# Performance work log

Hardware: AMD Instinct MI355X
Metric: run time of the kernel (lower is better)

Reference implementation:

```python
import jax, jax.numpy as jnp
import numpy as np

N, H, W, C = 8, 64, 64, 256
G, KS = 4, 3
K = KS * KS                      # 9 kernel points (remove_center=False)
GD = C // G                      # 64 channels per group
OM_DIM = int(np.ceil(G * K * 3 / 8) * 8)   # 112 = offsets(72)+mask(36)+pad(4)
STRIDE = PAD = DIL = 1
OFFSET_SCALE = 1.0
SOFTMAX = False


def setup_inputs() -> dict:
    ks = jax.random.split(jax.random.key(0), 6)
    s = 0.02
    return {
        "x": jax.random.normal(ks[0], (N, H * W, C), jnp.float32),
        "shape_h": H,
        "shape_w": W,
        "w_in": jax.random.normal(ks[1], (C, C), jnp.float32) * s,
        "b_in": jnp.zeros((C,), jnp.float32),
        "w_out": jax.random.normal(ks[2], (C, C), jnp.float32) * s,
        "b_out": jnp.zeros((C,), jnp.float32),
        "w_dw": jax.random.normal(ks[3], (KS, KS, 1, C), jnp.float32) * s,  # depthwise HWIO
        "b_dw": jnp.zeros((C,), jnp.float32),
        "w_pw": jax.random.normal(ks[4], (OM_DIM, C), jnp.float32) * s,
        "b_pw": jnp.zeros((OM_DIM,), jnp.float32),
    }


def _deform_sample(xg, px, py, mask):
    # xg: [N, H*W, G, GD]; px/py/mask: [N, H, W, G, K]
    # Bilinear sample with zero padding outside the image, mask-weighted sum over K.
    n_idx = jnp.arange(N)[:, None, None, None, None]
    g_idx = jnp.arange(G)[None, None, None, :, None]
    x0 = jnp.floor(px)
    y0 = jnp.floor(py)
    out = jnp.zeros((N, H, W, G, GD), xg.dtype)
    for dy in (0, 1):
        for dx in (0, 1):
            xi = x0 + dx
            yi = y0 + dy
            wgt = (1.0 - jnp.abs(px - xi)) * (1.0 - jnp.abs(py - yi))
            valid = (xi >= 0) & (xi <= W - 1) & (yi >= 0) & (yi <= H - 1)
            wgt = jnp.where(valid, wgt, 0.0) * mask                     # [N,H,W,G,K]
            flat = (jnp.clip(yi, 0, H - 1) * W + jnp.clip(xi, 0, W - 1)).astype(jnp.int32)
            vals = xg[n_idx, flat, g_idx, :]                            # [N,H,W,G,K,GD]
            out = out + jnp.einsum("nhwgk,nhwgkc->nhwgc", wgt, vals)
    return out


def _forward(x, w_in, b_in, w_out, b_out, w_dw, b_dw, w_pw, b_pw):
    out = x @ w_in.T + b_in                                             # proj_input [N,L,C]
    # offset/mask branch runs on the raw (unprojected) input
    dw = jax.lax.conv_general_dilated(
        x.reshape(N, H, W, C), w_dw, (1, 1), [(PAD, PAD), (PAD, PAD)],
        dimension_numbers=("NHWC", "HWIO", "NHWC"), feature_group_count=C) + b_dw
    om = (dw.reshape(N, H * W, C) @ w_pw.T + b_pw).reshape(N, H, W, OM_DIM)
    off = om[..., : 2 * G * K].reshape(N, H, W, G, K, 2)                # (dx, dy)
    mask = om[..., 2 * G * K : 3 * G * K].reshape(N, H, W, G, K)
    if SOFTMAX:
        mask = jax.nn.softmax(mask, axis=-1)
    # sampling locations in input pixel coordinates (DCNv3 reference points)
    kk = (jnp.arange(KS) - (KS - 1) // 2) * DIL
    kgy, kgx = jnp.meshgrid(kk, kk, indexing="ij")
    kgx = kgx.reshape(-1).astype(x.dtype)                               # [K]
    kgy = kgy.reshape(-1).astype(x.dtype)
    base = (DIL * (KS - 1)) // 2 - PAD
    bx = (jnp.arange(W) * STRIDE + base).astype(x.dtype)
    by = (jnp.arange(H) * STRIDE + base).astype(x.dtype)
    px = bx[None, None, :, None, None] + OFFSET_SCALE * (kgx + off[..., 0])
    py = by[None, :, None, None, None] + OFFSET_SCALE * (kgy + off[..., 1])
    samp = _deform_sample(out.reshape(N, H * W, G, GD), px, py, mask)   # [N,H,W,G,GD]
    return samp.reshape(N, H * W, C) @ w_out.T + b_out                  # proj_output


def reference(x, shape_h, shape_w, w_in, b_in, w_out, b_out, w_dw, b_dw, w_pw, b_pw):
    assert (shape_h, shape_w) == (H, W)
    return _forward(x, w_in, b_in, w_out, b_out, w_dw, b_dw, w_pw, b_pw)
```

## Files before the change

kernel.cpp:

```cpp
#include <hip/hip_runtime.h>

#define HW     4096
#define M_ROWS 32768
#define OMD    112
#define OMP    128

typedef __attribute__((ext_vector_type(8))) short short8;
typedef __attribute__((ext_vector_type(4))) float f32x4;

__device__ inline unsigned short f2bf(float f) {
  union { float f; unsigned int u; } v; v.f = f;
  unsigned int u = v.u;
  u += 0x7fffu + ((u >> 16) & 1u);
  return (unsigned short)(u >> 16);
}
__device__ inline float bf2f(unsigned short h) {
  union { unsigned int u; float f; } v; v.u = ((unsigned int)h) << 16;
  return v.f;
}

__global__ __launch_bounds__(256) void prep_fused(
    const float* __restrict__ x, const float* __restrict__ w_dw,
    const float* __restrict__ b_dw, const float* __restrict__ w_in,
    const float* __restrict__ w_out, const float* __restrict__ w_pw,
    const float* __restrict__ b_pw, unsigned short* __restrict__ xb,
    unsigned short* __restrict__ dwb, unsigned short* __restrict__ wi_b,
    unsigned short* __restrict__ wo_b, unsigned short* __restrict__ wp_b,
    float* __restrict__ bpw_pad) {
  int bid = blockIdx.x;
  int tid = threadIdx.x;
  if (bid < 8192) {
    int idx = bid * 256 + tid;
    int c4 = (idx & 63) * 4;
    int pp = idx >> 6;
    int n = pp >> 12;
    int hw = pp & 4095;
    int h = hw >> 6, w = hw & 63;
    float4 bb = *(const float4*)&b_dw[c4];
    float a0 = bb.x, a1 = bb.y, a2 = bb.z, a3 = bb.w;
#pragma unroll
    for (int ky = 0; ky < 3; ++ky) {
      int iy = h + ky - 1;
      if (iy < 0 || iy > 63) continue;
#pragma unroll
      for (int kx = 0; kx < 3; ++kx) {
        int ix = w + kx - 1;
        if (ix < 0 || ix > 63) continue;
        float4 xv = *(const float4*)&x[((size_t)(n << 12) + iy * 64 + ix) * 256 + c4];
        float4 wv = *(const float4*)&w_dw[(ky * 3 + kx) * 256 + c4];
        a0 += xv.x * wv.x;
        a1 += xv.y * wv.y;
        a2 += xv.z * wv.z;
        a3 += xv.w * wv.w;
      }
    }
    ushort4 o;
    o.x = f2bf(a0); o.y = f2bf(a1); o.z = f2bf(a2); o.w = f2bf(a3);
    *(ushort4*)&dwb[(size_t)pp * 256 + c4] = o;
    float4 cv = *(const float4*)&x[(size_t)pp * 256 + c4];
    ushort4 oc;
    oc.x = f2bf(cv.x); oc.y = f2bf(cv.y); oc.z = f2bf(cv.z); oc.w = f2bf(cv.w);
    *(ushort4*)&xb[(size_t)pp * 256 + c4] = oc;
  } else {
    int idx = (bid - 8192) * 256 + tid;
    if (idx < 65536) {
      wi_b[idx] = f2bf(w_in[idx]);
    } else if (idx < 131072) {
      int i = idx - 65536;
      wo_b[i] = f2bf(w_out[i]);
    } else if (idx < 131072 + OMP * 256) {
      int i = idx - 131072;
      int o = i >> 8;
      wp_b[i] = (o < OMD) ? f2bf(w_pw[i]) : (unsigned short)0;
    } else if (idx < 131072 + OMP * 256 + OMP) {
      int i = idx - (131072 + OMP * 256);
      bpw_pad[i] = (i < OMD) ? b_pw[i] : 0.f;
    }
  }
}

__global__ __launch_bounds__(256) void gemm_mid(
    const unsigned short* __restrict__ dwb, const unsigned short* __restrict__ wp_b,
    const float* __restrict__ bpw, unsigned short* __restrict__ om,
    const unsigned short* __restrict__ xb, const unsigned short* __restrict__ wi_b,
    const float* __restrict__ b_in, unsigned short* __restrict__ vproj) {
  __shared__ __align__(16) unsigned short As[128 * 32];
  __shared__ __align__(16) unsigned short Bs[128 * 32];
  int tid = threadIdx.x;
  int wave = tid >> 6, lane = tid & 63;
  int wr = wave >> 1, wc = wave & 1;

  const unsigned short *A, *W;
  const float* bias;
  unsigned short* Cout;
  int NN, colB;
  size_t rowB;
  int bid = blockIdx.x;
  if (bid < 256) {
    int swz = (bid & 7) * 32 + (bid >> 3);
    A = dwb; W = wp_b; bias = bpw; Cout = om; NN = 128;
    rowB = (size_t)swz * 128; colB = 0;
  } else {
    int b = bid - 256;
    int swz = (b & 7) * 64 + (b >> 3);
    A = xb; W = wi_b; bias = b_in; Cout = vproj; NN = 256;
    rowB = (size_t)(swz >> 1) * 128; colB = (swz & 1) * 128;
  }

  f32x4 acc[4][4];
#pragma unroll
  for (int m = 0; m < 4; ++m)
#pragma unroll
    for (int n = 0; n < 4; ++n) acc[m][n] = (f32x4)(0.f);

  int arow = lane >> 2;
  int acol = (lane & 3) * 8;

  for (int k0 = 0; k0 < 256; k0 += 32) {
#pragma unroll
    for (int jj = 0; jj < 2; ++jj) {
      int j = wave * 2 + jj;
      const unsigned short* ga = A + (rowB + 16 * j + arow) * 256 + k0 + acol;
      __builtin_amdgcn_global_load_lds(
          (const __attribute__((address_space(1))) unsigned int*)ga,
          (__attribute__((address_space(3))) unsigned int*)(As + j * 512),
          16, 0, 0);
      const unsigned short* gb =
          W + ((size_t)(colB + 16 * j + arow)) * 256 + k0 + acol;
      __builtin_amdgcn_global_load_lds(
          (const __attribute__((address_space(1))) unsigned int*)gb,
          (__attribute__((address_space(3))) unsigned int*)(Bs + j * 512),
          16, 0, 0);
    }
    __syncthreads();

    short8 aF[4], bF[4];
#pragma unroll
    for (int m = 0; m < 4; ++m)
      aF[m] = *(const short8*)&As[(wr * 64 + m * 16 + (lane & 15)) * 32 +
                                  (lane >> 4) * 8];
#pragma unroll
    for (int n = 0; n < 4; ++n)
      bF[n] = *(const short8*)&Bs[(wc * 64 + n * 16 + (lane & 15)) * 32 +
                                  (lane >> 4) * 8];
#pragma unroll
    for (int m = 0; m < 4; ++m)
#pragma unroll
      for (int n = 0; n < 4; ++n)
        acc[m][n] = __builtin_amdgcn_mfma_f32_16x16x32_bf16(
            aF[m], bF[n], acc[m][n], 0, 0, 0);
    __syncthreads();
  }

#pragma unroll
  for (int n = 0; n < 4; ++n) {
    int col = colB + wc * 64 + n * 16 + (lane & 15);
    float bv = bias[col];
#pragma unroll
    for (int m = 0; m < 4; ++m) {
#pragma unroll
      for (int j = 0; j < 4; ++j) {
        size_t row = rowB + wr * 64 + m * 16 + (lane >> 4) * 4 + j;
        Cout[row * NN + col] = f2bf(acc[m][n][j] + bv);
      }
    }
  }
}

__global__ __launch_bounds__(256) void gemm_out(
    const unsigned short* __restrict__ A, const unsigned short* __restrict__ W,
    const float* __restrict__ bias, float* __restrict__ Cout) {
  __shared__ __align__(16) unsigned short As[128 * 32];
  __shared__ __align__(16) unsigned short Bs[128 * 32];
  int tid = threadIdx.x;
  int wave = tid >> 6, lane = tid & 63;
  int wr = wave >> 1, wc = wave & 1;

  int bid = blockIdx.x;
  int swz = (bid & 7) * 64 + (bid >> 3);
  size_t rowB = (size_t)(swz >> 1) * 128;
  int colB = (swz & 1) * 128;

  f32x4 acc[4][4];
#pragma unroll
  for (int m = 0; m < 4; ++m)
#pragma unroll
    for (int n = 0; n < 4; ++n) acc[m][n] = (f32x4)(0.f);

  int arow = lane >> 2;
  int acol = (lane & 3) * 8;

  for (int k0 = 0; k0 < 256; k0 += 32) {
#pragma unroll
    for (int jj = 0; jj < 2; ++jj) {
      int j = wave * 2 + jj;
      const unsigned short* ga = A + (rowB + 16 * j + arow) * 256 + k0 + acol;
      __builtin_amdgcn_global_load_lds(
          (const __attribute__((address_space(1))) unsigned int*)ga,
          (__attribute__((address_space(3))) unsigned int*)(As + j * 512),
          16, 0, 0);
      const unsigned short* gb =
          W + ((size_t)(colB + 16 * j + arow)) * 256 + k0 + acol;
      __builtin_amdgcn_global_load_lds(
          (const __attribute__((address_space(1))) unsigned int*)gb,
          (__attribute__((address_space(3))) unsigned int*)(Bs + j * 512),
          16, 0, 0);
    }
    __syncthreads();

    short8 aF[4], bF[4];
#pragma unroll
    for (int m = 0; m < 4; ++m)
      aF[m] = *(const short8*)&As[(wr * 64 + m * 16 + (lane & 15)) * 32 +
                                  (lane >> 4) * 8];
#pragma unroll
    for (int n = 0; n < 4; ++n)
      bF[n] = *(const short8*)&Bs[(wc * 64 + n * 16 + (lane & 15)) * 32 +
                                  (lane >> 4) * 8];
#pragma unroll
    for (int m = 0; m < 4; ++m)
#pragma unroll
      for (int n = 0; n < 4; ++n)
        acc[m][n] = __builtin_amdgcn_mfma_f32_16x16x32_bf16(
            aF[m], bF[n], acc[m][n], 0, 0, 0);
    __syncthreads();
  }

#pragma unroll
  for (int n = 0; n < 4; ++n) {
    int col = colB + wc * 64 + n * 16 + (lane & 15);
    float bv = bias[col];
#pragma unroll
    for (int m = 0; m < 4; ++m) {
#pragma unroll
      for (int j = 0; j < 4; ++j) {
        size_t row = rowB + wr * 64 + m * 16 + (lane >> 4) * 4 + j;
        Cout[row * 256 + col] = acc[m][n][j] + bv;
      }
    }
  }
}

__global__ __launch_bounds__(256) void deform_sample_b3(
    const unsigned short* __restrict__ vproj, const unsigned short* __restrict__ om,
    unsigned short* __restrict__ samp) {
  int bid = blockIdx.x;
  int swz = (bid & 7) * 512 + (bid >> 3);
  int p0 = swz * 8;

  int tid = threadIdx.x;

  __shared__ __align__(16) float s_w[8][36][4];
  __shared__ __align__(16) int   s_o[8][36][4];

  for (int it = tid; it < 288; it += 256) {
    int pix = it / 36, gk = it % 36;
    int k = gk % 9;
    int p = p0 + pix;
    int h = (p >> 6) & 63, w = p & 63;
    const unsigned short* o = om + (size_t)p * OMP;
    float ox = bf2f(o[gk * 2]), oy = bf2f(o[gk * 2 + 1]);
    float m = bf2f(o[72 + gk]);
    float px = (float)(w + (k % 3) - 1) + ox;
    float py = (float)(h + (k / 3) - 1) + oy;
    float x0f = floorf(px), y0f = floorf(py);
    int x0 = (int)x0f, y0 = (int)y0f;
    float fx = px - x0f, fy = py - y0f;
    bool vx0 = (unsigned)x0 < 64u;
    bool vx1 = (unsigned)(x0 + 1) < 64u;
    bool vy0 = (unsigned)y0 < 64u;
    bool vy1 = (unsigned)(y0 + 1) < 64u;
    s_w[pix][gk][0] = (vy0 && vx0) ? (1.f - fx) * (1.f - fy) * m : 0.f;
    s_w[pix][gk][1] = (vy0 && vx1) ? fx * (1.f - fy) * m : 0.f;
    s_w[pix][gk][2] = (vy1 && vx0) ? (1.f - fx) * fy * m : 0.f;
    s_w[pix][gk][3] = (vy1 && vx1) ? fx * fy * m : 0.f;
    int x0c = min(max(x0, 0), 63), x1c = min(max(x0 + 1, 0), 63);
    int y0c = min(max(y0, 0), 63), y1c = min(max(y0 + 1, 0), 63);
    s_o[pix][gk][0] = (y0c * 64 + x0c) * 512;
    s_o[pix][gk][1] = (y0c * 64 + x1c) * 512;
    s_o[pix][gk][2] = (y1c * 64 + x0c) * 512;
    s_o[pix][gk][3] = (y1c * 64 + x1c) * 512;
  }
  __syncthreads();

  int wave = tid >> 6, lane = tid & 63;
  int pix2 = lane >> 5, sub = lane & 31, g = sub >> 3;
  int pixb = wave * 2 + pix2;
  int p = p0 + pixb;
  int n = p0 >> 12;
  const char* vb = (const char*)(vproj + (((size_t)n << 12)) * 256);
  int choff = sub * 16;

  float acc[8];
#pragma unroll
  for (int j = 0; j < 8; ++j) acc[j] = 0.f;

#pragma unroll
  for (int k = 0; k < 9; ++k) {
    int gk = g * 9 + k;
    float4 wv = *(const float4*)s_w[pixb][gk];
    int4 ov = *(const int4*)s_o[pixb][gk];
#pragma unroll
    for (int c = 0; c < 4; ++c) {
      int off = (c == 0) ? ov.x : (c == 1) ? ov.y : (c == 2) ? ov.z : ov.w;
      float wgt = (c == 0) ? wv.x : (c == 1) ? wv.y : (c == 2) ? wv.z : wv.w;
      short8 v = *(const short8*)(vb + off + choff);
#pragma unroll
      for (int j = 0; j < 8; ++j)
        acc[j] += wgt * bf2f((unsigned short)v[j]);
    }
  }

  union { unsigned short s[8]; short8 v8; } o;
#pragma unroll
  for (int j = 0; j < 8; ++j) o.s[j] = f2bf(acc[j]);
  *(short8*)&samp[(size_t)p * 256 + sub * 8] = o.v8;
}

extern "C" void kernel_launch(void* const* d_in, const int* in_sizes, int n_in,
                              void* d_out, int out_size, void* d_ws,
                              size_t ws_size, hipStream_t stream) {
  const float* x     = (const float*)d_in[0];
  const float* w_in  = (const float*)d_in[3];
  const float* b_in  = (const float*)d_in[4];
  const float* w_out = (const float*)d_in[5];
  const float* b_out = (const float*)d_in[6];
  const float* w_dw  = (const float*)d_in[7];
  const float* b_dw  = (const float*)d_in[8];
  const float* w_pw  = (const float*)d_in[9];
  const float* b_pw  = (const float*)d_in[10];
  float* out = (float*)d_out;
  char* ws = (char*)d_ws;

  unsigned short* xb    = (unsigned short*)(ws);
  unsigned short* dwb   = (unsigned short*)(ws + (16u << 20));
  unsigned short* vproj = (unsigned short*)(ws + (32u << 20));
  unsigned short* om    = (unsigned short*)(ws + (48u << 20));
  unsigned short* wi_b  = (unsigned short*)(ws + (56u << 20));
  unsigned short* wo_b  = (unsigned short*)(ws + (56u << 20) + (128u << 10));
  unsigned short* wp_b  = (unsigned short*)(ws + (56u << 20) + (256u << 10));
  float*          bpw   = (float*)(ws + (56u << 20) + (320u << 10));

  prep_fused<<<8834, 256, 0, stream>>>(x, w_dw, b_dw, w_in, w_out, w_pw, b_pw,
                                       xb, dwb, wi_b, wo_b, wp_b, bpw);
  gemm_mid<<<768, 256, 0, stream>>>(dwb, wp_b, bpw, om, xb, wi_b, b_in, vproj);
  deform_sample_b3<<<4096, 256, 0, stream>>>(vproj, om, dwb );
  gemm_out<<<512, 256, 0, stream>>>(dwb, wo_b, b_out, out);
}
```

Baseline: 80.81 us.

## Fuse deformable sampling into output projection GEMM via shared memory tile

Merges the bilinear deform-sampling kernel with the output projection GEMM. Each block samples 64 pixels into a padded LDS tile, then multiplies it against the full 256-column weight matrix with MFMA. This removes the bf16 round trip of the sampled tensor through global memory and one kernel launch. In exchange the grid shrinks to 512 blocks, the sampling phase has less parallelism per block, and every block reloads all of W.

```diff
diff --git a/kernel.cpp b/kernel.cpp
--- a/kernel.cpp
+++ b/kernel.cpp
@@ -167,43 +167,90 @@
   }
 }
 
-__global__ __launch_bounds__(256) void gemm_out(
-    const unsigned short* __restrict__ A, const unsigned short* __restrict__ W,
-    const float* __restrict__ bias, float* __restrict__ Cout) {
-  __shared__ __align__(16) unsigned short As[128 * 32];
-  __shared__ __align__(16) unsigned short Bs[128 * 32];
+__global__ __launch_bounds__(256) void fused_sample_gemm(
+    const unsigned short* __restrict__ vproj, const unsigned short* __restrict__ om,
+    const unsigned short* __restrict__ W, const float* __restrict__ bias,
+    float* __restrict__ out) {
+  constexpr int AP = 264;
+  __shared__ __align__(16) unsigned short As[64 * AP];
+  __shared__ __align__(16) unsigned short Bs[256 * 32];
+
+  int bid = blockIdx.x;
+  int swz = (bid & 7) * 64 + (bid >> 3);
+  int p0 = swz * 64;
+  int n = p0 >> 12;
+
   int tid = threadIdx.x;
   int wave = tid >> 6, lane = tid & 63;
-  int wr = wave >> 1, wc = wave & 1;
-
-  int bid = blockIdx.x;
-  int swz = (bid & 7) * 64 + (bid >> 3);
-  size_t rowB = (size_t)(swz >> 1) * 128;
-  int colB = (swz & 1) * 128;
-
-  f32x4 acc[4][4];
+  int pix2 = lane >> 5, sub = lane & 31, g = sub >> 3;
+
+  const char* vb_img = (const char*)(vproj + (((size_t)n << 12)) * 256);
+  int choff = sub * 16;
+
+  for (int iter = 0; iter < 8; ++iter) {
+    int pl = wave * 16 + iter * 2 + pix2;
+    int p = p0 + pl;
+    int hy = (p >> 6) & 63, wx = p & 63;
+    const unsigned short* o = om + (size_t)p * OMP;
+
+    float acc[8];
+#pragma unroll
+    for (int j = 0; j < 8; ++j) acc[j] = 0.f;
+
+#pragma unroll
+    for (int k = 0; k < 9; ++k) {
+      int gk = g * 9 + k;
+      float ox = bf2f(o[gk * 2]), oy = bf2f(o[gk * 2 + 1]);
+      float msk = bf2f(o[72 + gk]);
+      float px = (float)(wx + (k % 3) - 1) + ox;
+      float py = (float)(hy + (k / 3) - 1) + oy;
+      float x0f = floorf(px), y0f = floorf(py);
+      int x0 = (int)x0f, y0 = (int)y0f;
+      float fx = px - x0f, fy = py - y0f;
+      bool vx0 = (unsigned)x0 < 64u, vx1 = (unsigned)(x0 + 1) < 64u;
+      bool vy0 = (unsigned)y0 < 64u, vy1 = (unsigned)(y0 + 1) < 64u;
+      float w00 = (vy0 && vx0) ? (1.f - fx) * (1.f - fy) * msk : 0.f;
+      float w01 = (vy0 && vx1) ? fx * (1.f - fy) * msk : 0.f;
+      float w10 = (vy1 && vx0) ? (1.f - fx) * fy * msk : 0.f;
+      float w11 = (vy1 && vx1) ? fx * fy * msk : 0.f;
+      int x0c = min(max(x0, 0), 63), x1c = min(max(x0 + 1, 0), 63);
+      int y0c = min(max(y0, 0), 63), y1c = min(max(y0 + 1, 0), 63);
+      const char* r0 = vb_img + y0c * 32768 + choff;
+      const char* r1 = vb_img + y1c * 32768 + choff;
+      short8 v00 = *(const short8*)(r0 + x0c * 512);
+      short8 v01 = *(const short8*)(r0 + x1c * 512);
+      short8 v10 = *(const short8*)(r1 + x0c * 512);
+      short8 v11 = *(const short8*)(r1 + x1c * 512);
+#pragma unroll
+      for (int j = 0; j < 8; ++j)
+        acc[j] += w00 * bf2f((unsigned short)v00[j]) +
+                  w01 * bf2f((unsigned short)v01[j]) +
+                  w10 * bf2f((unsigned short)v10[j]) +
+                  w11 * bf2f((unsigned short)v11[j]);
+    }
+
+    union { unsigned short s[8]; short8 v8; } o8;
+#pragma unroll
+    for (int j = 0; j < 8; ++j) o8.s[j] = f2bf(acc[j]);
+    *(short8*)&As[pl * AP + sub * 8] = o8.v8;
+  }
+  __syncthreads();
+
+  f32x4 acc2[4][4];
 #pragma unroll
   for (int m = 0; m < 4; ++m)
 #pragma unroll
-    for (int n = 0; n < 4; ++n) acc[m][n] = (f32x4)(0.f);
-
-  int arow = lane >> 2;
-  int acol = (lane & 3) * 8;
-
-  for (int k0 = 0; k0 < 256; k0 += 32) {
-#pragma unroll
-    for (int jj = 0; jj < 2; ++jj) {
-      int j = wave * 2 + jj;
-      const unsigned short* ga = A + (rowB + 16 * j + arow) * 256 + k0 + acol;
-      __builtin_amdgcn_global_load_lds(
-          (const __attribute__((address_space(1))) unsigned int*)ga,
-          (__attribute__((address_space(3))) unsigned int*)(As + j * 512),
-          16, 0, 0);
+    for (int nn = 0; nn < 4; ++nn) acc2[m][nn] = (f32x4)(0.f);
+
+  for (int j = 0; j < 8; ++j) {
+#pragma unroll
+    for (int jj = 0; jj < 4; ++jj) {
+      int r = wave * 4 + jj;
       const unsigned short* gb =
-          W + ((size_t)(colB + 16 * j + arow)) * 256 + k0 + acol;
+          W + ((size_t)(16 * r + (lane >> 2))) * 256 + j * 32 + (lane & 3) * 8;
       __builtin_amdgcn_global_load_lds(
           (const __attribute__((address_space(1))) unsigned int*)gb,
-          (__attribute__((address_space(3))) unsigned int*)(Bs + j * 512),
+          (__attribute__((address_space(3))) unsigned int*)(Bs + r * 512),
           16, 0, 0);
     }
     __syncthreads();
@@ -211,110 +258,34 @@
     short8 aF[4], bF[4];
 #pragma unroll
     for (int m = 0; m < 4; ++m)
-      aF[m] = *(const short8*)&As[(wr * 64 + m * 16 + (lane & 15)) * 32 +
+      aF[m] = *(const short8*)&As[(m * 16 + (lane & 15)) * AP + j * 32 +
                                   (lane >> 4) * 8];
 #pragma unroll
-    for (int n = 0; n < 4; ++n)
-      bF[n] = *(const short8*)&Bs[(wc * 64 + n * 16 + (lane & 15)) * 32 +
-                                  (lane >> 4) * 8];
+    for (int nn = 0; nn < 4; ++nn)
+      bF[nn] = *(const short8*)&Bs[(wave * 64 + nn * 16 + (lane & 15)) * 32 +
+                                   (lane >> 4) * 8];
 #pragma unroll
     for (int m = 0; m < 4; ++m)
 #pragma unroll
-      for (int n = 0; n < 4; ++n)
-        acc[m][n] = __builtin_amdgcn_mfma_f32_16x16x32_bf16(
-            aF[m], bF[n], acc[m][n], 0, 0, 0);
+      for (int nn = 0; nn < 4; ++nn)
+        acc2[m][nn] = __builtin_amdgcn_mfma_f32_16x16x32_bf16(
+            aF[m], bF[nn], acc2[m][nn], 0, 0, 0);
     __syncthreads();
   }
 
 #pragma unroll
-  for (int n = 0; n < 4; ++n) {
-    int col = colB + wc * 64 + n * 16 + (lane & 15);
+  for (int nn = 0; nn < 4; ++nn) {
+    int col = wave * 64 + nn * 16 + (lane & 15);
     float bv = bias[col];
 #pragma unroll
     for (int m = 0; m < 4; ++m) {
 #pragma unroll
-      for (int j = 0; j < 4; ++j) {
-        size_t row = rowB + wr * 64 + m * 16 + (lane >> 4) * 4 + j;
-        Cout[row * 256 + col] = acc[m][n][j] + bv;
+      for (int jr = 0; jr < 4; ++jr) {
+        size_t row = (size_t)p0 + m * 16 + (lane >> 4) * 4 + jr;
+        out[row * 256 + col] = acc2[m][nn][jr] + bv;
       }
     }
   }
-}
-
-__global__ __launch_bounds__(256) void deform_sample_b3(
-    const unsigned short* __restrict__ vproj, const unsigned short* __restrict__ om,
-    unsigned short* __restrict__ samp) {
-  int bid = blockIdx.x;
-  int swz = (bid & 7) * 512 + (bid >> 3);
-  int p0 = swz * 8;
-
-  int tid = threadIdx.x;
-
-  __shared__ __align__(16) float s_w[8][36][4];
-  __shared__ __align__(16) int   s_o[8][36][4];
-
-  for (int it = tid; it < 288; it += 256) {
-    int pix = it / 36, gk = it % 36;
-    int k = gk % 9;
-    int p = p0 + pix;
-    int h = (p >> 6) & 63, w = p & 63;
-    const unsigned short* o = om + (size_t)p * OMP;
-    float ox = bf2f(o[gk * 2]), oy = bf2f(o[gk * 2 + 1]);
-    float m = bf2f(o[72 + gk]);
-    float px = (float)(w + (k % 3) - 1) + ox;
-    float py = (float)(h + (k / 3) - 1) + oy;
-    float x0f = floorf(px), y0f = floorf(py);
-    int x0 = (int)x0f, y0 = (int)y0f;
-    float fx = px - x0f, fy = py - y0f;
-    bool vx0 = (unsigned)x0 < 64u;
-    bool vx1 = (unsigned)(x0 + 1) < 64u;
-    bool vy0 = (unsigned)y0 < 64u;
-    bool vy1 = (unsigned)(y0 + 1) < 64u;
-    s_w[pix][gk][0] = (vy0 && vx0) ? (1.f - fx) * (1.f - fy) * m : 0.f;
-    s_w[pix][gk][1] = (vy0 && vx1) ? fx * (1.f - fy) * m : 0.f;
-    s_w[pix][gk][2] = (vy1 && vx0) ? (1.f - fx) * fy * m : 0.f;
-    s_w[pix][gk][3] = (vy1 && vx1) ? fx * fy * m : 0.f;
-    int x0c = min(max(x0, 0), 63), x1c = min(max(x0 + 1, 0), 63);
-    int y0c = min(max(y0, 0), 63), y1c = min(max(y0 + 1, 0), 63);
-    s_o[pix][gk][0] = (y0c * 64 + x0c) * 512;
-    s_o[pix][gk][1] = (y0c * 64 + x1c) * 512;
-    s_o[pix][gk][2] = (y1c * 64 + x0c) * 512;
-    s_o[pix][gk][3] = (y1c * 64 + x1c) * 512;
-  }
-  __syncthreads();
-
-  int wave = tid >> 6, lane = tid & 63;
-  int pix2 = lane >> 5, sub = lane & 31, g = sub >> 3;
-  int pixb = wave * 2 + pix2;
-  int p = p0 + pixb;
-  int n = p0 >> 12;
-  const char* vb = (const char*)(vproj + (((size_t)n << 12)) * 256);
-  int choff = sub * 16;
-
-  float acc[8];
-#pragma unroll
-  for (int j = 0; j < 8; ++j) acc[j] = 0.f;
-
-#pragma unroll
-  for (int k = 0; k < 9; ++k) {
-    int gk = g * 9 + k;
-    float4 wv = *(const float4*)s_w[pixb][gk];
-    int4 ov = *(const int4*)s_o[pixb][gk];
-#pragma unroll
-    for (int c = 0; c < 4; ++c) {
-      int off = (c == 0) ? ov.x : (c == 1) ? ov.y : (c == 2) ? ov.z : ov.w;
-      float wgt = (c == 0) ? wv.x : (c == 1) ? wv.y : (c == 2) ? wv.z : wv.w;
-      short8 v = *(const short8*)(vb + off + choff);
-#pragma unroll
-      for (int j = 0; j < 8; ++j)
-        acc[j] += wgt * bf2f((unsigned short)v[j]);
-    }
-  }
-
-  union { unsigned short s[8]; short8 v8; } o;
-#pragma unroll
-  for (int j = 0; j < 8; ++j) o.s[j] = f2bf(acc[j]);
-  *(short8*)&samp[(size_t)p * 256 + sub * 8] = o.v8;
 }
 
 extern "C" void kernel_launch(void* const* d_in, const int* in_sizes, int n_in,
@@ -344,6 +315,5 @@
   prep_fused<<<8834, 256, 0, stream>>>(x, w_dw, b_dw, w_in, w_out, w_pw, b_pw,
                                        xb, dwb, wi_b, wo_b, wp_b, bpw);
   gemm_mid<<<768, 256, 0, stream>>>(dwb, wp_b, bpw, om, xb, wi_b, b_in, vproj);
-  deform_sample_b3<<<4096, 256, 0, stream>>>(vproj, om, dwb );
-  gemm_out<<<512, 256, 0, stream>>>(dwb, wo_b, b_out, out);
-}
+  fused_sample_gemm<<<512, 256, 0, stream>>>(vproj, om, wo_b, b_out, out);
+}
```

Result: slower. 100.2 us (+24.0%).
